# Optimization experiments

Hardware: AMD Instinct MI355X
Metric: run time of the kernel (lower is better)

## Reference

```python
import jax, jax.numpy as jnp
import numpy as np

N = 100000
E = 1600000
IN = 128
HID = 128
OUT = 40
EPS = 1e-5
NEG_SLOPE = 0.2


def _gat_layer(x, src, dst, W, a_src, a_dst, b, heads, out_dim):
    # x: [N, in]; W: [in, heads*out_dim]; a_src/a_dst: [heads, out_dim]; b: [heads*out_dim]
    n = x.shape[0]
    h = (x @ W).reshape(n, heads, out_dim)                      # [N, H, D]
    al_s = jnp.sum(h * a_src, axis=-1)                          # [N, H]
    al_d = jnp.sum(h * a_dst, axis=-1)                          # [N, H]
    e = jax.nn.leaky_relu(al_s[src] + al_d[dst], NEG_SLOPE)     # [E, H]
    m = jax.ops.segment_max(e, dst, num_segments=n)             # [N, H]
    m = jnp.where(jnp.isfinite(m), m, 0.0)
    ex = jnp.exp(e - m[dst])                                    # [E, H]
    denom = jax.ops.segment_sum(ex, dst, num_segments=n)        # [N, H]
    alpha = ex / (denom[dst] + 1e-16)                           # [E, H]
    out = jax.ops.segment_sum(alpha[:, :, None] * h[src], dst, num_segments=n)  # [N, H, D]
    return out.reshape(n, heads * out_dim) + b


def _bn(h, g, beta):
    mu = jnp.mean(h, axis=0)
    var = jnp.var(h, axis=0)
    return (h - mu) * jax.lax.rsqrt(var + EPS) * g + beta


def setup_inputs() -> dict:
    key = jax.random.key(0)
    ks = jax.random.split(key, 20)
    x = jax.random.normal(ks[0], (N, IN), dtype=jnp.float32)
    edge_index = jax.random.randint(ks[1], (2, E), 0, N, dtype=jnp.int64)
    s = 0.05
    d0 = HID // 2  # 64, heads=2
    return {
        "x": x,
        "edge_index": edge_index,
        "w0": jax.random.normal(ks[2], (IN, 2 * d0), jnp.float32) * s,
        "asrc0": jax.random.normal(ks[3], (2, d0), jnp.float32) * s,
        "adst0": jax.random.normal(ks[4], (2, d0), jnp.float32) * s,
        "b0": jnp.zeros((2 * d0,), jnp.float32),
        "g0": jnp.ones((2 * d0,), jnp.float32),
        "beta0": jnp.zeros((2 * d0,), jnp.float32),
        "w1": jax.random.normal(ks[5], (HID, 2 * d0), jnp.float32) * s,
        "asrc1": jax.random.normal(ks[6], (2, d0), jnp.float32) * s,
        "adst1": jax.random.normal(ks[7], (2, d0), jnp.float32) * s,
        "b1": jnp.zeros((2 * d0,), jnp.float32),
        "g1": jnp.ones((2 * d0,), jnp.float32),
        "beta1": jnp.zeros((2 * d0,), jnp.float32),
        "w2": jax.random.normal(ks[8], (HID, OUT), jnp.float32) * s,
        "asrc2": jax.random.normal(ks[9], (1, OUT), jnp.float32) * s,
        "adst2": jax.random.normal(ks[10], (1, OUT), jnp.float32) * s,
        "b2": jnp.zeros((OUT,), jnp.float32),
    }


def reference(x, edge_index, w0, asrc0, adst0, b0, g0, beta0,
              w1, asrc1, adst1, b1, g1, beta1,
              w2, asrc2, adst2, b2):
    src, dst = edge_index[0], edge_index[1]
    d0 = HID // 2
    # layer 0: GATConv(IN, 64, heads=2) -> BN -> ReLU (dropout off in eval)
    h = _gat_layer(x, src, dst, w0, asrc0, adst0, b0, 2, d0)
    h = jax.nn.relu(_bn(h, g0, beta0))
    # layer 1
    h = _gat_layer(h, src, dst, w1, asrc1, adst1, b1, 2, d0)
    h = jax.nn.relu(_bn(h, g1, beta1))
    # layer 2: GATConv(HID, OUT, heads=1), no bn/relu
    h = _gat_layer(h, src, dst, w2, asrc2, adst2, b2, 1, OUT)
    return h
```

## Files before the change

### kernel.cpp

```cpp
#include <hip/hip_runtime.h>
#include <cstdint>


#define TILE_A 8192
#define BCAP 10240
#define NSLICE 32

typedef __attribute__((ext_vector_type(8))) short bf16x8v;
typedef __attribute__((ext_vector_type(4))) float f32x4v;
typedef __attribute__((ext_vector_type(2))) float f32x2;
typedef __attribute__((ext_vector_type(2))) unsigned int u32x2;

__device__ __forceinline__ uint32_t bf16x2_pack(float a, float b) {
  uint32_t ua = __float_as_uint(a);
  ua = (ua + 0x7FFF + ((ua >> 16) & 1)) >> 16;
  uint32_t ub = __float_as_uint(b);
  ub = (ub + 0x7FFF + ((ub >> 16) & 1)) >> 16;
  return ua | (ub << 16);
}
__device__ __forceinline__ uint16_t bf16_1(float a) {
  uint32_t ua = __float_as_uint(a);
  return (uint16_t)((ua + 0x7FFF + ((ua >> 16) & 1)) >> 16);
}
__device__ __forceinline__ f32x2 up2(uint32_t u) {
  u32x2 t = {u << 16, u & 0xFFFF0000u};
  return __builtin_bit_cast(f32x2, t);
}


__global__ __launch_bounds__(256) void bucket_hist_k(const int* __restrict__ dst,
                                                     int* __restrict__ counts,
                                                     int E, int nbA, int nbuck) {
  __shared__ int hist[256];
  int t = threadIdx.x;
  hist[t] = 0;
  __syncthreads();
  int lo = blockIdx.x * TILE_A;
  int hi = min(lo + TILE_A, E);
  for (int i = lo + t; i < hi; i += 256) atomicAdd(&hist[dst[i] >> 9], 1);
  __syncthreads();
  if (t < nbuck) counts[t * nbA + blockIdx.x] = hist[t];
}

__global__ __launch_bounds__(1024) void scan_counts_k(int* __restrict__ counts, int M,
                                                      int* __restrict__ rowptr, int N, int E) {
  __shared__ int part[1024];
  int t = threadIdx.x;
  int chunk = (M + 1023) >> 10;
  int lo = t * chunk, hi = min(lo + chunk, M);
  int s = 0;
  for (int i = lo; i < hi; ++i) s += counts[i];
  part[t] = s;
  __syncthreads();
  for (int off = 1; off < 1024; off <<= 1) {
    int u = (t >= off) ? part[t - off] : 0;
    __syncthreads();
    part[t] += u;
    __syncthreads();
  }
  int run = (t == 0) ? 0 : part[t - 1];
  for (int i = lo; i < hi; ++i) {
    int v = counts[i];
    counts[i] = run;
    run += v;
  }
  if (t == 0) rowptr[N] = E;
}

__global__ __launch_bounds__(256) void bucket_scatter_k(const int* __restrict__ src,
                                                        const int* __restrict__ dst,
                                                        const int* __restrict__ counts,
                                                        uint32_t* __restrict__ barr,
                                                        int E, int nbA, int nbuck) {
  __shared__ int cur[256];
  int t = threadIdx.x;
  if (t < nbuck) cur[t] = counts[t * nbA + blockIdx.x];
  __syncthreads();
  int lo = blockIdx.x * TILE_A;
  int hi = min(lo + TILE_A, E);
  for (int i = lo + t; i < hi; i += 256) {
    int d = dst[i];
    int b = d >> 9;
    int pos = atomicAdd(&cur[b], 1);
    barr[pos] = ((uint32_t)(d & 511) << 17) | (uint32_t)src[i];
  }
}

__global__ __launch_bounds__(256) void bucket_sort_k(const uint32_t* __restrict__ barr,
                                                     const int* __restrict__ counts,
                                                     int* __restrict__ rowptr,
                                                     int* __restrict__ csr_src,
                                                     int nbA, int nbuck, int N, int E) {
  __shared__ uint32_t ebuf[BCAP];
  __shared__ int hist[512];
  __shared__ int cur[512];
  int b = blockIdx.x;
  int t = threadIdx.x;
  int start = counts[b * nbA];
  int end = (b == nbuck - 1) ? E : counts[(b + 1) * nbA];
  int cnt = end - start;
  if (cnt > BCAP) cnt = BCAP;
  for (int i = t; i < cnt; i += 256) ebuf[i] = barr[start + i];
  for (int i = t; i < 512; i += 256) hist[i] = 0;
  __syncthreads();
  for (int i = t; i < cnt; i += 256) atomicAdd(&hist[ebuf[i] >> 17], 1);
  __syncthreads();
  if (t < 64) {
    int v[8];
    int s = 0;
#pragma unroll
    for (int k = 0; k < 8; ++k) { v[k] = hist[t * 8 + k]; s += v[k]; }
    int inc = s;
#pragma unroll
    for (int off = 1; off < 64; off <<= 1) {
      int u = __shfl_up(inc, off, 64);
      if (t >= off) inc += u;
    }
    int run = inc - s;
#pragma unroll
    for (int k = 0; k < 8; ++k) { hist[t * 8 + k] = run; run += v[k]; }
  }
  __syncthreads();
  int node0 = b << 9;
  int lim = N - node0;
  if (lim > 512) lim = 512;
  for (int i = t; i < 512; i += 256) {
    cur[i] = hist[i];
    if (i < lim) rowptr[node0 + i] = start + hist[i];
  }
  __syncthreads();
  for (int i = t; i < cnt; i += 256) {
    uint32_t e = ebuf[i];
    int ld = e >> 17;
    int pos = atomicAdd(&cur[ld], 1);
    csr_src[start + pos] = (int)(e & 0x1FFFFu);
  }
}


__global__ void w_prep_all_k(const float* __restrict__ w0, const float* __restrict__ w1,
                             const float* __restrict__ w2, uint16_t* __restrict__ wt0,
                             uint16_t* __restrict__ wt1, uint16_t* __restrict__ wt2) {
  int idx = blockIdx.x * blockDim.x + threadIdx.x;
  if (idx < 16384) {
    int n = idx >> 7, k = idx & 127;
    wt0[idx] = bf16_1(w0[k * 128 + n]);
  } else if (idx < 32768) {
    int i = idx - 16384;
    int n = i >> 7, k = i & 127;
    wt1[i] = bf16_1(w1[k * 128 + n]);
  } else if (idx < 32768 + 48 * 128) {
    int i = idx - 32768;
    int n = i >> 7, k = i & 127;
    float v = (n < 40) ? w2[k * 40 + n] : 0.f;
    wt2[i] = bf16_1(v);
  }
}

template <bool NORM, int NT, int HEADS>
__global__ __launch_bounds__(256) void gemm_mfma_k(const float* __restrict__ X,
                                                   const uint16_t* __restrict__ WT,
                                                   uint16_t* __restrict__ Hout,
                                                   const float* __restrict__ stats,
                                                   const float* __restrict__ g,
                                                   const float* __restrict__ beta,
                                                   const float* __restrict__ asrc,
                                                   const float* __restrict__ adst,
                                                   float* __restrict__ als,
                                                   float* __restrict__ ald,
                                                   int nrows, int cols) {
  __shared__ short A_lds[64 * 136];
  __shared__ float sscale[128];
  __shared__ float sbias[128];
  int tid = threadIdx.x;
  if (NORM && tid < 128) {
    float s = 0.f, s2 = 0.f;
#pragma unroll 4
    for (int sl = 0; sl < NSLICE; ++sl) {
      s += stats[sl * 256 + tid];
      s2 += stats[sl * 256 + 128 + tid];
    }
    float invn = 1.0f / (float)nrows;
    float mean = s * invn;
    float var = s2 * invn - mean * mean;
    float sc = g[tid] * rsqrtf(var + 1e-5f);
    sscale[tid] = sc;
    sbias[tid] = beta[tid] - mean * sc;
  }
  if (NORM) __syncthreads();
  int row0 = blockIdx.x * 64;
#pragma unroll
  for (int it = 0; it < 8; ++it) {
    int e = (tid + it * 256) * 4;
    int row = e >> 7;
    int kh = e & 127;
    int gr = row0 + row;
    float4 xv = make_float4(0.f, 0.f, 0.f, 0.f);
    if (gr < nrows) xv = *(const float4*)(X + (size_t)gr * 128 + kh);
    if (NORM) {
      xv.x = fmaxf(fmaf(xv.x, sscale[kh + 0], sbias[kh + 0]), 0.f);
      xv.y = fmaxf(fmaf(xv.y, sscale[kh + 1], sbias[kh + 1]), 0.f);
      xv.z = fmaxf(fmaf(xv.z, sscale[kh + 2], sbias[kh + 2]), 0.f);
      xv.w = fmaxf(fmaf(xv.w, sscale[kh + 3], sbias[kh + 3]), 0.f);
    }
    uint2 pk;
    pk.x = bf16x2_pack(xv.x, xv.y);
    pk.y = bf16x2_pack(xv.z, xv.w);
    *(uint2*)(&A_lds[row * 136 + kh]) = pk;
  }
  __syncthreads();

  int wave = tid >> 6;
  int lane = tid & 63;
  int m = lane & 15;
  int quad = lane >> 4;

  bf16x8v afrag[4];
#pragma unroll
  for (int kc = 0; kc < 4; ++kc)
    afrag[kc] = *(const bf16x8v*)(&A_lds[(wave * 16 + m) * 136 + kc * 32 + quad * 8]);

  f32x4v acc[NT];
#pragma unroll
  for (int t = 0; t < NT; ++t) acc[t] = (f32x4v){0.f, 0.f, 0.f, 0.f};

#pragma unroll
  for (int t = 0; t < NT; ++t) {
#pragma unroll
    for (int kc = 0; kc < 4; ++kc) {
      bf16x8v bfrag = *(const bf16x8v*)(WT + ((t * 16 + m) * 128 + kc * 32 + quad * 8));
      acc[t] = __builtin_amdgcn_mfma_f32_16x16x32_bf16(afrag[kc], bfrag, acc[t], 0, 0, 0);
    }
  }

#pragma unroll
  for (int t = 0; t < NT; ++t) {
    int col = t * 16 + m;
    if (col >= cols) break;
#pragma unroll
    for (int r = 0; r < 4; ++r) {
      int row = row0 + wave * 16 + quad * 4 + r;
      if (row < nrows) Hout[(size_t)row * cols + col] = bf16_1(acc[t][r]);
    }
  }

  float as_v[NT], ad_v[NT];
#pragma unroll
  for (int t = 0; t < NT; ++t) {
    int col = t * 16 + m;
    as_v[t] = (col < cols) ? asrc[col] : 0.f;
    ad_v[t] = (col < cols) ? adst[col] : 0.f;
  }
#pragma unroll
  for (int r = 0; r < 4; ++r) {
    int row = row0 + wave * 16 + quad * 4 + r;
    if (HEADS == 2) {
      float s1h0 = 0.f, s2h0 = 0.f, s1h1 = 0.f, s2h1 = 0.f;
#pragma unroll
      for (int t = 0; t < NT / 2; ++t) {
        s1h0 += acc[t][r] * as_v[t];
        s2h0 += acc[t][r] * ad_v[t];
      }
#pragma unroll
      for (int t = NT / 2; t < NT; ++t) {
        s1h1 += acc[t][r] * as_v[t];
        s2h1 += acc[t][r] * ad_v[t];
      }
#pragma unroll
      for (int off = 1; off < 16; off <<= 1) {
        s1h0 += __shfl_xor(s1h0, off, 64);
        s2h0 += __shfl_xor(s2h0, off, 64);
        s1h1 += __shfl_xor(s1h1, off, 64);
        s2h1 += __shfl_xor(s2h1, off, 64);
      }
      if (m == 0 && row < nrows) {
        ((float2*)als)[row] = make_float2(s1h0, s1h1);
        ((float2*)ald)[row] = make_float2(s2h0, s2h1);
      }
    } else {
      float s1 = 0.f, s2 = 0.f;
#pragma unroll
      for (int t = 0; t < NT; ++t) {
        s1 += acc[t][r] * as_v[t];
        s2 += acc[t][r] * ad_v[t];
      }
#pragma unroll
      for (int off = 1; off < 16; off <<= 1) {
        s1 += __shfl_xor(s1, off, 64);
        s2 += __shfl_xor(s2, off, 64);
      }
      if (m == 0 && row < nrows) {
        als[row] = s1;
        ald[row] = s2;
      }
    }
  }
}

__global__ __launch_bounds__(256) void gat_gather2_k(const int* __restrict__ rowptr,
                                                     const int* __restrict__ csr_src,
                                                     const float* __restrict__ als,
                                                     const float* __restrict__ ald,
                                                     const uint16_t* __restrict__ H,
                                                     const float* __restrict__ bias,
                                                     float* __restrict__ out,
                                                     float* __restrict__ stats, int N) {
  __shared__ float red[4][256];
  int tid = threadIdx.x;
  int wv = tid >> 6;
  int n = blockIdx.x * 4 + wv;
  int lane = tid & 63;
  int slot = lane >> 4;
  int sub = lane & 15;
  int head = sub >> 3;
  bool alive = n < N;
  int start = 0, end = 0;
  float aldn = 0.f;
  if (alive) {
    start = rowptr[n];
    end = rowptr[n + 1];
    aldn = ald[2 * n + head];
  }
  const char* hbase = (const char*)H;
  uint32_t suboff = (uint32_t)sub << 4;
  bool dlane = (sub & 7) == 0;
  f32x2 acc0 = {0.f, 0.f}, acc1 = {0.f, 0.f}, acc2 = {0.f, 0.f}, acc3 = {0.f, 0.f};
  float dsum = 0.f;
  int j = start;
  for (; j + 16 <= end; j += 16) {
    int e0 = j + slot;
    int s0 = csr_src[e0];
    int s1 = csr_src[e0 + 4];
    int s2 = csr_src[e0 + 8];
    int s3 = csr_src[e0 + 12];
    uint4 u0 = *(const uint4*)(hbase + (((uint32_t)s0 << 8) + suboff));
    uint4 u1 = *(const uint4*)(hbase + (((uint32_t)s1 << 8) + suboff));
    uint4 u2 = *(const uint4*)(hbase + (((uint32_t)s2 << 8) + suboff));
    uint4 u3 = *(const uint4*)(hbase + (((uint32_t)s3 << 8) + suboff));
    float l0 = als[2 * s0 + head] + aldn;
    float l1 = als[2 * s1 + head] + aldn;
    float l2 = als[2 * s2 + head] + aldn;
    float l3 = als[2 * s3 + head] + aldn;
    l0 = fmaxf(l0, 0.2f * l0);
    l1 = fmaxf(l1, 0.2f * l1);
    l2 = fmaxf(l2, 0.2f * l2);
    l3 = fmaxf(l3, 0.2f * l3);
    float w0 = __expf(l0), w1 = __expf(l1), w2 = __expf(l2), w3 = __expf(l3);
    if (dlane) dsum += (w0 + w1) + (w2 + w3);
    acc0 += up2(u0.x) * w0;
    acc1 += up2(u0.y) * w0;
    acc2 += up2(u0.z) * w0;
    acc3 += up2(u0.w) * w0;
    acc0 += up2(u1.x) * w1;
    acc1 += up2(u1.y) * w1;
    acc2 += up2(u1.z) * w1;
    acc3 += up2(u1.w) * w1;
    acc0 += up2(u2.x) * w2;
    acc1 += up2(u2.y) * w2;
    acc2 += up2(u2.z) * w2;
    acc3 += up2(u2.w) * w2;
    acc0 += up2(u3.x) * w3;
    acc1 += up2(u3.y) * w3;
    acc2 += up2(u3.z) * w3;
    acc3 += up2(u3.w) * w3;
  }
  for (; j < end; j += 8) {
    int last = end - 1;
    int ea = j + slot;
    int eb = ea + 4;
    int sa = csr_src[min(ea, last)];
    int sb = csr_src[min(eb, last)];
    uint4 ua = *(const uint4*)(hbase + (((uint32_t)sa << 8) + suboff));
    uint4 ub = *(const uint4*)(hbase + (((uint32_t)sb << 8) + suboff));
    float la = als[2 * sa + head] + aldn;
    float lb = als[2 * sb + head] + aldn;
    la = fmaxf(la, 0.2f * la);
    lb = fmaxf(lb, 0.2f * lb);
    float wa = (ea < end) ? __expf(la) : 0.f;
    float wb = (eb < end) ? __expf(lb) : 0.f;
    if (dlane) dsum += wa + wb;
    acc0 += up2(ua.x) * wa;
    acc1 += up2(ua.y) * wa;
    acc2 += up2(ua.z) * wa;
    acc3 += up2(ua.w) * wa;
    acc0 += up2(ub.x) * wb;
    acc1 += up2(ub.y) * wb;
    acc2 += up2(ub.z) * wb;
    acc3 += up2(ub.w) * wb;
  }
  acc0.x += __shfl_xor(acc0.x, 16, 64); acc0.x += __shfl_xor(acc0.x, 32, 64);
  acc0.y += __shfl_xor(acc0.y, 16, 64); acc0.y += __shfl_xor(acc0.y, 32, 64);
  acc1.x += __shfl_xor(acc1.x, 16, 64); acc1.x += __shfl_xor(acc1.x, 32, 64);
  acc1.y += __shfl_xor(acc1.y, 16, 64); acc1.y += __shfl_xor(acc1.y, 32, 64);
  acc2.x += __shfl_xor(acc2.x, 16, 64); acc2.x += __shfl_xor(acc2.x, 32, 64);
  acc2.y += __shfl_xor(acc2.y, 16, 64); acc2.y += __shfl_xor(acc2.y, 32, 64);
  acc3.x += __shfl_xor(acc3.x, 16, 64); acc3.x += __shfl_xor(acc3.x, 32, 64);
  acc3.y += __shfl_xor(acc3.y, 16, 64); acc3.y += __shfl_xor(acc3.y, 32, 64);
  dsum += __shfl_xor(dsum, 16, 64);
  dsum += __shfl_xor(dsum, 32, 64);
  float denom = __shfl(dsum, head << 3, 64);
  if (slot == 0) {
    float inv = 1.0f / (denom + 1e-16f);
    float4 b0 = ((const float4*)bias)[2 * sub];
    float4 b1 = ((const float4*)bias)[2 * sub + 1];
    float4 o0, o1;
    o0.x = acc0.x * inv + b0.x;
    o0.y = acc0.y * inv + b0.y;
    o0.z = acc1.x * inv + b0.z;
    o0.w = acc1.y * inv + b0.w;
    o1.x = acc2.x * inv + b1.x;
    o1.y = acc2.y * inv + b1.y;
    o1.z = acc3.x * inv + b1.z;
    o1.w = acc3.y * inv + b1.w;
    if (alive) {
      ((float4*)out)[(size_t)n * 32 + 2 * sub] = o0;
      ((float4*)out)[(size_t)n * 32 + 2 * sub + 1] = o1;
    }
    float z = alive ? 1.f : 0.f;
    int c = sub << 3;
    red[wv][c + 0] = o0.x * z;  red[wv][128 + c + 0] = o0.x * o0.x * z;
    red[wv][c + 1] = o0.y * z;  red[wv][128 + c + 1] = o0.y * o0.y * z;
    red[wv][c + 2] = o0.z * z;  red[wv][128 + c + 2] = o0.z * o0.z * z;
    red[wv][c + 3] = o0.w * z;  red[wv][128 + c + 3] = o0.w * o0.w * z;
    red[wv][c + 4] = o1.x * z;  red[wv][128 + c + 4] = o1.x * o1.x * z;
    red[wv][c + 5] = o1.y * z;  red[wv][128 + c + 5] = o1.y * o1.y * z;
    red[wv][c + 6] = o1.z * z;  red[wv][128 + c + 6] = o1.z * o1.z * z;
    red[wv][c + 7] = o1.w * z;  red[wv][128 + c + 7] = o1.w * o1.w * z;
  }
  __syncthreads();
  float v = red[0][tid] + red[1][tid] + red[2][tid] + red[3][tid];
  atomicAdd(&stats[((blockIdx.x & (NSLICE - 1)) << 8) + tid], v);
}

__global__ __launch_bounds__(256) void gat_gather1_k(const int* __restrict__ rowptr,
                                                     const int* __restrict__ csr_src,
                                                     const float* __restrict__ als,
                                                     const float* __restrict__ ald,
                                                     const uint16_t* __restrict__ H,
                                                     const float* __restrict__ bias,
                                                     float* __restrict__ out, int N) {
  int n = blockIdx.x * 4 + (threadIdx.x >> 6);
  if (n >= N) return;
  int lane = threadIdx.x & 63;
  int slot = lane / 5;
  int d = lane - slot * 5;
  bool act = slot < 12;
  int start = rowptr[n], end = rowptr[n + 1];
  float aldn = ald[n];
  const char* hbase = (const char*)H;
  uint32_t doff = (uint32_t)d << 4;
  f32x2 a0 = {0.f, 0.f}, a1 = {0.f, 0.f}, a2 = {0.f, 0.f}, a3 = {0.f, 0.f};
  float dsum = 0.f;
  for (int j = start; j < end; j += 24) {
    int last = end - 1;
    int e0 = j + slot;
    int e1 = e0 + 12;
    int s0 = act ? csr_src[min(e0, last)] : 0;
    int s1 = act ? csr_src[min(e1, last)] : 0;
    uint4 u0 = *(const uint4*)(hbase + ((uint32_t)s0 * 80u + doff));
    uint4 u1 = *(const uint4*)(hbase + ((uint32_t)s1 * 80u + doff));
    float l0 = als[s0] + aldn;
    float l1 = als[s1] + aldn;
    l0 = fmaxf(l0, 0.2f * l0);
    l1 = fmaxf(l1, 0.2f * l1);
    float w0 = (act && e0 < end) ? __expf(l0) : 0.f;
    float w1 = (act && e1 < end) ? __expf(l1) : 0.f;
    if (d == 0) dsum += w0 + w1;
    a0 += up2(u0.x) * w0;
    a1 += up2(u0.y) * w0;
    a2 += up2(u0.z) * w0;
    a3 += up2(u0.w) * w0;
    a0 += up2(u1.x) * w1;
    a1 += up2(u1.y) * w1;
    a2 += up2(u1.z) * w1;
    a3 += up2(u1.w) * w1;
  }
#define FOLD2(off)                                        \
  a0.x += __shfl(a0.x, (lane + off) & 63, 64);            \
  a0.y += __shfl(a0.y, (lane + off) & 63, 64);            \
  a1.x += __shfl(a1.x, (lane + off) & 63, 64);            \
  a1.y += __shfl(a1.y, (lane + off) & 63, 64);            \
  a2.x += __shfl(a2.x, (lane + off) & 63, 64);            \
  a2.y += __shfl(a2.y, (lane + off) & 63, 64);            \
  a3.x += __shfl(a3.x, (lane + off) & 63, 64);            \
  a3.y += __shfl(a3.y, (lane + off) & 63, 64);
  FOLD2(30)
  FOLD2(15)
  {
    float t;
    t = __shfl(a0.x, (lane + 5) & 63, 64) + __shfl(a0.x, (lane + 10) & 63, 64); a0.x += t;
    t = __shfl(a0.y, (lane + 5) & 63, 64) + __shfl(a0.y, (lane + 10) & 63, 64); a0.y += t;
    t = __shfl(a1.x, (lane + 5) & 63, 64) + __shfl(a1.x, (lane + 10) & 63, 64); a1.x += t;
    t = __shfl(a1.y, (lane + 5) & 63, 64) + __shfl(a1.y, (lane + 10) & 63, 64); a1.y += t;
    t = __shfl(a2.x, (lane + 5) & 63, 64) + __shfl(a2.x, (lane + 10) & 63, 64); a2.x += t;
    t = __shfl(a2.y, (lane + 5) & 63, 64) + __shfl(a2.y, (lane + 10) & 63, 64); a2.y += t;
    t = __shfl(a3.x, (lane + 5) & 63, 64) + __shfl(a3.x, (lane + 10) & 63, 64); a3.x += t;
    t = __shfl(a3.y, (lane + 5) & 63, 64) + __shfl(a3.y, (lane + 10) & 63, 64); a3.y += t;
  }
#undef FOLD2
#pragma unroll
  for (int off = 1; off < 64; off <<= 1) dsum += __shfl_xor(dsum, off, 64);
  if (lane < 5) {
    float inv = 1.0f / (dsum + 1e-16f);
    float4 b4a = ((const float4*)bias)[2 * d];
    float4 b4b = ((const float4*)bias)[2 * d + 1];
    float4 o0, o1;
    o0.x = a0.x * inv + b4a.x;
    o0.y = a0.y * inv + b4a.y;
    o0.z = a1.x * inv + b4a.z;
    o0.w = a1.y * inv + b4a.w;
    o1.x = a2.x * inv + b4b.x;
    o1.y = a2.y * inv + b4b.y;
    o1.z = a3.x * inv + b4b.z;
    o1.w = a3.y * inv + b4b.w;
    float* orow = out + (size_t)n * 40 + 8 * d;
    *(float4*)orow = o0;
    *(float4*)(orow + 4) = o1;
  }
}

extern "C" void kernel_launch(void* const* d_in, const int* in_sizes, int n_in,
                              void* d_out, int out_size, void* d_ws, size_t ws_size,
                              hipStream_t stream) {
  const float* x     = (const float*)d_in[0];
  const int*   ei    = (const int*)d_in[1];
  const float* w0    = (const float*)d_in[2];
  const float* asrc0 = (const float*)d_in[3];
  const float* adst0 = (const float*)d_in[4];
  const float* b0    = (const float*)d_in[5];
  const float* g0    = (const float*)d_in[6];
  const float* beta0 = (const float*)d_in[7];
  const float* w1    = (const float*)d_in[8];
  const float* asrc1 = (const float*)d_in[9];
  const float* adst1 = (const float*)d_in[10];
  const float* b1    = (const float*)d_in[11];
  const float* g1    = (const float*)d_in[12];
  const float* beta1 = (const float*)d_in[13];
  const float* w2    = (const float*)d_in[14];
  const float* asrc2 = (const float*)d_in[15];
  const float* adst2 = (const float*)d_in[16];
  const float* b2    = (const float*)d_in[17];

  const int N = in_sizes[0] / 128;
  const int E = in_sizes[1] / 2;

  const int nbuck = (N + 511) >> 9;
  const int nbA = (E + TILE_A - 1) / TILE_A;

  char* p = (char*)d_ws;
  auto carve = [&](size_t bytes) {
    char* q = p;
    p += (bytes + 255) & ~(size_t)255;
    return q;
  };
  int*      counts  = (int*)carve((size_t)nbuck * nbA * 4);
  int*      rowptr  = (int*)carve((size_t)(N + 1) * 4);
  uint32_t* barr    = (uint32_t*)carve((size_t)E * 4);
  int*      csr_src = (int*)carve((size_t)E * 4);
  float*    als     = (float*)carve((size_t)N * 2 * 4);
  float*    ald     = (float*)carve((size_t)N * 2 * 4);
  float*    stats   = (float*)carve((size_t)NSLICE * 256 * 4);
  uint16_t* wt0     = (uint16_t*)carve(128 * 128 * 2);
  uint16_t* wt1     = (uint16_t*)carve(128 * 128 * 2);
  uint16_t* wt2     = (uint16_t*)carve(48 * 128 * 2);
  uint16_t* hbuf    = (uint16_t*)carve((size_t)N * 128 * 2);
  float*    agg     = (float*)carve((size_t)N * 128 * 4);

  const int* esrc = ei;
  const int* edst = ei + E;

  bucket_hist_k<<<nbA, 256, 0, stream>>>(edst, counts, E, nbA, nbuck);
  scan_counts_k<<<1, 1024, 0, stream>>>(counts, nbuck * nbA, rowptr, N, E);
  bucket_scatter_k<<<nbA, 256, 0, stream>>>(esrc, edst, counts, barr, E, nbA, nbuck);
  bucket_sort_k<<<nbuck, 256, 0, stream>>>(barr, counts, rowptr, csr_src, nbA, nbuck, N, E);

  w_prep_all_k<<<(32768 + 48 * 128 + 255) / 256, 256, 0, stream>>>(w0, w1, w2, wt0, wt1, wt2);

  const int gemm_grid = (N + 63) / 64;
  const int node_grid = (N + 3) / 4;

  gemm_mfma_k<false, 8, 2><<<gemm_grid, 256, 0, stream>>>(x, wt0, hbuf, nullptr, nullptr,
                                                          nullptr, asrc0, adst0, als, ald,
                                                          N, 128);
  hipMemsetAsync(stats, 0, NSLICE * 256 * 4, stream);
  gat_gather2_k<<<node_grid, 256, 0, stream>>>(rowptr, csr_src, als, ald, hbuf,
                                               b0, agg, stats, N);

  gemm_mfma_k<true, 8, 2><<<gemm_grid, 256, 0, stream>>>(agg, wt1, hbuf, stats, g0, beta0,
                                                         asrc1, adst1, als, ald, N, 128);
  hipMemsetAsync(stats, 0, NSLICE * 256 * 4, stream);
  gat_gather2_k<<<node_grid, 256, 0, stream>>>(rowptr, csr_src, als, ald, hbuf,
                                               b1, agg, stats, N);

  gemm_mfma_k<true, 3, 1><<<gemm_grid, 256, 0, stream>>>(agg, wt2, hbuf, stats, g1, beta1,
                                                         asrc2, adst2, als, ald, N, 40);
  gat_gather1_k<<<node_grid, 256, 0, stream>>>(rowptr, csr_src, als, ald, hbuf,
                                               b2, (float*)d_out, N);
}
```

Measured before the change: 532.6 us.

## Process eight nodes per wave in gather and use nontemporal loads/stores

The two-head gather kernel now gives each wave 8 consecutive destination nodes instead of one. It keeps BatchNorm partial sums in registers across those nodes, so there is one LDS reduction and one stats atomic pass per block instead of per node, and the grid shrinks 8x. Streaming accesses (csr_src reads, GEMM input reads, output writes) switch to nontemporal builtins to reduce cache pollution for the gathered H rows. The cost is fewer waves in flight for hiding latency on the irregular gathers, and more serial work per wave.

```diff
diff --git a/kernel.cpp b/kernel.cpp
--- a/kernel.cpp
+++ b/kernel.cpp
@@ -195,17 +195,17 @@
     int row = e >> 7;
     int kh = e & 127;
     int gr = row0 + row;
-    float4 xv = make_float4(0.f, 0.f, 0.f, 0.f);
-    if (gr < nrows) xv = *(const float4*)(X + (size_t)gr * 128 + kh);
+    f32x4v xv = {0.f, 0.f, 0.f, 0.f};
+    if (gr < nrows) xv = __builtin_nontemporal_load((const f32x4v*)(X + (size_t)gr * 128 + kh));
     if (NORM) {
-      xv.x = fmaxf(fmaf(xv.x, sscale[kh + 0], sbias[kh + 0]), 0.f);
-      xv.y = fmaxf(fmaf(xv.y, sscale[kh + 1], sbias[kh + 1]), 0.f);
-      xv.z = fmaxf(fmaf(xv.z, sscale[kh + 2], sbias[kh + 2]), 0.f);
-      xv.w = fmaxf(fmaf(xv.w, sscale[kh + 3], sbias[kh + 3]), 0.f);
+      xv[0] = fmaxf(fmaf(xv[0], sscale[kh + 0], sbias[kh + 0]), 0.f);
+      xv[1] = fmaxf(fmaf(xv[1], sscale[kh + 1], sbias[kh + 1]), 0.f);
+      xv[2] = fmaxf(fmaf(xv[2], sscale[kh + 2], sbias[kh + 2]), 0.f);
+      xv[3] = fmaxf(fmaf(xv[3], sscale[kh + 3], sbias[kh + 3]), 0.f);
     }
     uint2 pk;
-    pk.x = bf16x2_pack(xv.x, xv.y);
-    pk.y = bf16x2_pack(xv.z, xv.w);
+    pk.x = bf16x2_pack(xv[0], xv[1]);
+    pk.y = bf16x2_pack(xv[2], xv[3]);
     *(uint2*)(&A_lds[row * 136 + kh]) = pk;
   }
   __syncthreads();
@@ -308,124 +308,137 @@
   __shared__ float red[4][256];
   int tid = threadIdx.x;
   int wv = tid >> 6;
-  int n = blockIdx.x * 4 + wv;
   int lane = tid & 63;
   int slot = lane >> 4;
   int sub = lane & 15;
   int head = sub >> 3;
-  bool alive = n < N;
-  int start = 0, end = 0;
-  float aldn = 0.f;
-  if (alive) {
-    start = rowptr[n];
-    end = rowptr[n + 1];
-    aldn = ald[2 * n + head];
-  }
   const char* hbase = (const char*)H;
   uint32_t suboff = (uint32_t)sub << 4;
   bool dlane = (sub & 7) == 0;
-  f32x2 acc0 = {0.f, 0.f}, acc1 = {0.f, 0.f}, acc2 = {0.f, 0.f}, acc3 = {0.f, 0.f};
-  float dsum = 0.f;
-  int j = start;
-  for (; j + 16 <= end; j += 16) {
-    int e0 = j + slot;
-    int s0 = csr_src[e0];
-    int s1 = csr_src[e0 + 4];
-    int s2 = csr_src[e0 + 8];
-    int s3 = csr_src[e0 + 12];
-    uint4 u0 = *(const uint4*)(hbase + (((uint32_t)s0 << 8) + suboff));
-    uint4 u1 = *(const uint4*)(hbase + (((uint32_t)s1 << 8) + suboff));
-    uint4 u2 = *(const uint4*)(hbase + (((uint32_t)s2 << 8) + suboff));
-    uint4 u3 = *(const uint4*)(hbase + (((uint32_t)s3 << 8) + suboff));
-    float l0 = als[2 * s0 + head] + aldn;
-    float l1 = als[2 * s1 + head] + aldn;
-    float l2 = als[2 * s2 + head] + aldn;
-    float l3 = als[2 * s3 + head] + aldn;
-    l0 = fmaxf(l0, 0.2f * l0);
-    l1 = fmaxf(l1, 0.2f * l1);
-    l2 = fmaxf(l2, 0.2f * l2);
-    l3 = fmaxf(l3, 0.2f * l3);
-    float w0 = __expf(l0), w1 = __expf(l1), w2 = __expf(l2), w3 = __expf(l3);
-    if (dlane) dsum += (w0 + w1) + (w2 + w3);
-    acc0 += up2(u0.x) * w0;
-    acc1 += up2(u0.y) * w0;
-    acc2 += up2(u0.z) * w0;
-    acc3 += up2(u0.w) * w0;
-    acc0 += up2(u1.x) * w1;
-    acc1 += up2(u1.y) * w1;
-    acc2 += up2(u1.z) * w1;
-    acc3 += up2(u1.w) * w1;
-    acc0 += up2(u2.x) * w2;
-    acc1 += up2(u2.y) * w2;
-    acc2 += up2(u2.z) * w2;
-    acc3 += up2(u2.w) * w2;
-    acc0 += up2(u3.x) * w3;
-    acc1 += up2(u3.y) * w3;
-    acc2 += up2(u3.z) * w3;
-    acc3 += up2(u3.w) * w3;
-  }
-  for (; j < end; j += 8) {
-    int last = end - 1;
-    int ea = j + slot;
-    int eb = ea + 4;
-    int sa = csr_src[min(ea, last)];
-    int sb = csr_src[min(eb, last)];
-    uint4 ua = *(const uint4*)(hbase + (((uint32_t)sa << 8) + suboff));
-    uint4 ub = *(const uint4*)(hbase + (((uint32_t)sb << 8) + suboff));
-    float la = als[2 * sa + head] + aldn;
-    float lb = als[2 * sb + head] + aldn;
-    la = fmaxf(la, 0.2f * la);
-    lb = fmaxf(lb, 0.2f * lb);
-    float wa = (ea < end) ? __expf(la) : 0.f;
-    float wb = (eb < end) ? __expf(lb) : 0.f;
-    if (dlane) dsum += wa + wb;
-    acc0 += up2(ua.x) * wa;
-    acc1 += up2(ua.y) * wa;
-    acc2 += up2(ua.z) * wa;
-    acc3 += up2(ua.w) * wa;
-    acc0 += up2(ub.x) * wb;
-    acc1 += up2(ub.y) * wb;
-    acc2 += up2(ub.z) * wb;
-    acc3 += up2(ub.w) * wb;
-  }
-  acc0.x += __shfl_xor(acc0.x, 16, 64); acc0.x += __shfl_xor(acc0.x, 32, 64);
-  acc0.y += __shfl_xor(acc0.y, 16, 64); acc0.y += __shfl_xor(acc0.y, 32, 64);
-  acc1.x += __shfl_xor(acc1.x, 16, 64); acc1.x += __shfl_xor(acc1.x, 32, 64);
-  acc1.y += __shfl_xor(acc1.y, 16, 64); acc1.y += __shfl_xor(acc1.y, 32, 64);
-  acc2.x += __shfl_xor(acc2.x, 16, 64); acc2.x += __shfl_xor(acc2.x, 32, 64);
-  acc2.y += __shfl_xor(acc2.y, 16, 64); acc2.y += __shfl_xor(acc2.y, 32, 64);
-  acc3.x += __shfl_xor(acc3.x, 16, 64); acc3.x += __shfl_xor(acc3.x, 32, 64);
-  acc3.y += __shfl_xor(acc3.y, 16, 64); acc3.y += __shfl_xor(acc3.y, 32, 64);
-  dsum += __shfl_xor(dsum, 16, 64);
-  dsum += __shfl_xor(dsum, 32, 64);
-  float denom = __shfl(dsum, head << 3, 64);
+  int n0 = (blockIdx.x * 4 + wv) * 8;
+  float4 b0 = ((const float4*)bias)[2 * sub];
+  float4 b1 = ((const float4*)bias)[2 * sub + 1];
+  float ss[8], sq[8];
+#pragma unroll
+  for (int k = 0; k < 8; ++k) { ss[k] = 0.f; sq[k] = 0.f; }
+
+  for (int ni = 0; ni < 8; ++ni) {
+    int n = n0 + ni;
+    bool alive = n < N;
+    int start = 0, end = 0;
+    float aldn = 0.f;
+    if (alive) {
+      start = rowptr[n];
+      end = rowptr[n + 1];
+      aldn = ald[2 * n + head];
+    }
+    f32x2 acc0 = {0.f, 0.f}, acc1 = {0.f, 0.f}, acc2 = {0.f, 0.f}, acc3 = {0.f, 0.f};
+    float dsum = 0.f;
+    int j = start;
+    for (; j + 16 <= end; j += 16) {
+      int e0 = j + slot;
+      int s0 = __builtin_nontemporal_load(csr_src + e0);
+      int s1 = __builtin_nontemporal_load(csr_src + e0 + 4);
+      int s2 = __builtin_nontemporal_load(csr_src + e0 + 8);
+      int s3 = __builtin_nontemporal_load(csr_src + e0 + 12);
+      uint4 u0 = *(const uint4*)(hbase + (((uint32_t)s0 << 8) + suboff));
+      uint4 u1 = *(const uint4*)(hbase + (((uint32_t)s1 << 8) + suboff));
+      uint4 u2 = *(const uint4*)(hbase + (((uint32_t)s2 << 8) + suboff));
+      uint4 u3 = *(const uint4*)(hbase + (((uint32_t)s3 << 8) + suboff));
+      float l0 = als[2 * s0 + head] + aldn;
+      float l1 = als[2 * s1 + head] + aldn;
+      float l2 = als[2 * s2 + head] + aldn;
+      float l3 = als[2 * s3 + head] + aldn;
+      l0 = fmaxf(l0, 0.2f * l0);
+      l1 = fmaxf(l1, 0.2f * l1);
+      l2 = fmaxf(l2, 0.2f * l2);
+      l3 = fmaxf(l3, 0.2f * l3);
+      float w0 = __expf(l0), w1 = __expf(l1), w2 = __expf(l2), w3 = __expf(l3);
+      if (dlane) dsum += (w0 + w1) + (w2 + w3);
+      acc0 += up2(u0.x) * w0;
+      acc1 += up2(u0.y) * w0;
+      acc2 += up2(u0.z) * w0;
+      acc3 += up2(u0.w) * w0;
+      acc0 += up2(u1.x) * w1;
+      acc1 += up2(u1.y) * w1;
+      acc2 += up2(u1.z) * w1;
+      acc3 += up2(u1.w) * w1;
+      acc0 += up2(u2.x) * w2;
+      acc1 += up2(u2.y) * w2;
+      acc2 += up2(u2.z) * w2;
+      acc3 += up2(u2.w) * w2;
+      acc0 += up2(u3.x) * w3;
+      acc1 += up2(u3.y) * w3;
+      acc2 += up2(u3.z) * w3;
+      acc3 += up2(u3.w) * w3;
+    }
+    for (; j < end; j += 8) {
+      int last = end - 1;
+      int ea = j + slot;
+      int eb = ea + 4;
+      int sa = csr_src[min(ea, last)];
+      int sb = csr_src[min(eb, last)];
+      uint4 ua = *(const uint4*)(hbase + (((uint32_t)sa << 8) + suboff));
+      uint4 ub = *(const uint4*)(hbase + (((uint32_t)sb << 8) + suboff));
+      float la = als[2 * sa + head] + aldn;
+      float lb = als[2 * sb + head] + aldn;
+      la = fmaxf(la, 0.2f * la);
+      lb = fmaxf(lb, 0.2f * lb);
+      float wa = (ea < end) ? __expf(la) : 0.f;
+      float wb = (eb < end) ? __expf(lb) : 0.f;
+      if (dlane) dsum += wa + wb;
+      acc0 += up2(ua.x) * wa;
+      acc1 += up2(ua.y) * wa;
+      acc2 += up2(ua.z) * wa;
+      acc3 += up2(ua.w) * wa;
+      acc0 += up2(ub.x) * wb;
+      acc1 += up2(ub.y) * wb;
+      acc2 += up2(ub.z) * wb;
+      acc3 += up2(ub.w) * wb;
+    }
+    acc0.x += __shfl_xor(acc0.x, 16, 64); acc0.x += __shfl_xor(acc0.x, 32, 64);
+    acc0.y += __shfl_xor(acc0.y, 16, 64); acc0.y += __shfl_xor(acc0.y, 32, 64);
+    acc1.x += __shfl_xor(acc1.x, 16, 64); acc1.x += __shfl_xor(acc1.x, 32, 64);
+    acc1.y += __shfl_xor(acc1.y, 16, 64); acc1.y += __shfl_xor(acc1.y, 32, 64);
+    acc2.x += __shfl_xor(acc2.x, 16, 64); acc2.x += __shfl_xor(acc2.x, 32, 64);
+    acc2.y += __shfl_xor(acc2.y, 16, 64); acc2.y += __shfl_xor(acc2.y, 32, 64);
+    acc3.x += __shfl_xor(acc3.x, 16, 64); acc3.x += __shfl_xor(acc3.x, 32, 64);
+    acc3.y += __shfl_xor(acc3.y, 16, 64); acc3.y += __shfl_xor(acc3.y, 32, 64);
+    dsum += __shfl_xor(dsum, 16, 64);
+    dsum += __shfl_xor(dsum, 32, 64);
+    float denom = __shfl(dsum, head << 3, 64);
+    if (slot == 0 && alive) {
+      float inv = 1.0f / (denom + 1e-16f);
+      f32x4v o0, o1;
+      o0[0] = acc0.x * inv + b0.x;
+      o0[1] = acc0.y * inv + b0.y;
+      o0[2] = acc1.x * inv + b0.z;
+      o0[3] = acc1.y * inv + b0.w;
+      o1[0] = acc2.x * inv + b1.x;
+      o1[1] = acc2.y * inv + b1.y;
+      o1[2] = acc3.x * inv + b1.z;
+      o1[3] = acc3.y * inv + b1.w;
+      float* orow = out + (size_t)n * 128 + 8 * sub;
+      __builtin_nontemporal_store(o0, (f32x4v*)orow);
+      __builtin_nontemporal_store(o1, (f32x4v*)(orow + 4));
+      ss[0] += o0[0]; sq[0] += o0[0] * o0[0];
+      ss[1] += o0[1]; sq[1] += o0[1] * o0[1];
+      ss[2] += o0[2]; sq[2] += o0[2] * o0[2];
+      ss[3] += o0[3]; sq[3] += o0[3] * o0[3];
+      ss[4] += o1[0]; sq[4] += o1[0] * o1[0];
+      ss[5] += o1[1]; sq[5] += o1[1] * o1[1];
+      ss[6] += o1[2]; sq[6] += o1[2] * o1[2];
+      ss[7] += o1[3]; sq[7] += o1[3] * o1[3];
+    }
+  }
+
   if (slot == 0) {
-    float inv = 1.0f / (denom + 1e-16f);
-    float4 b0 = ((const float4*)bias)[2 * sub];
-    float4 b1 = ((const float4*)bias)[2 * sub + 1];
-    float4 o0, o1;
-    o0.x = acc0.x * inv + b0.x;
-    o0.y = acc0.y * inv + b0.y;
-    o0.z = acc1.x * inv + b0.z;
-    o0.w = acc1.y * inv + b0.w;
-    o1.x = acc2.x * inv + b1.x;
-    o1.y = acc2.y * inv + b1.y;
-    o1.z = acc3.x * inv + b1.z;
-    o1.w = acc3.y * inv + b1.w;
-    if (alive) {
-      ((float4*)out)[(size_t)n * 32 + 2 * sub] = o0;
-      ((float4*)out)[(size_t)n * 32 + 2 * sub + 1] = o1;
-    }
-    float z = alive ? 1.f : 0.f;
     int c = sub << 3;
-    red[wv][c + 0] = o0.x * z;  red[wv][128 + c + 0] = o0.x * o0.x * z;
-    red[wv][c + 1] = o0.y * z;  red[wv][128 + c + 1] = o0.y * o0.y * z;
-    red[wv][c + 2] = o0.z * z;  red[wv][128 + c + 2] = o0.z * o0.z * z;
-    red[wv][c + 3] = o0.w * z;  red[wv][128 + c + 3] = o0.w * o0.w * z;
-    red[wv][c + 4] = o1.x * z;  red[wv][128 + c + 4] = o1.x * o1.x * z;
-    red[wv][c + 5] = o1.y * z;  red[wv][128 + c + 5] = o1.y * o1.y * z;
-    red[wv][c + 6] = o1.z * z;  red[wv][128 + c + 6] = o1.z * o1.z * z;
-    red[wv][c + 7] = o1.w * z;  red[wv][128 + c + 7] = o1.w * o1.w * z;
+#pragma unroll
+    for (int k = 0; k < 8; ++k) {
+      red[wv][c + k] = ss[k];
+      red[wv][128 + c + k] = sq[k];
+    }
   }
   __syncthreads();
   float v = red[0][tid] + red[1][tid] + red[2][tid] + red[3][tid];
@@ -455,8 +468,8 @@
     int last = end - 1;
     int e0 = j + slot;
     int e1 = e0 + 12;
-    int s0 = act ? csr_src[min(e0, last)] : 0;
-    int s1 = act ? csr_src[min(e1, last)] : 0;
+    int s0 = act ? __builtin_nontemporal_load(csr_src + min(e0, last)) : 0;
+    int s1 = act ? __builtin_nontemporal_load(csr_src + min(e1, last)) : 0;
     uint4 u0 = *(const uint4*)(hbase + ((uint32_t)s0 * 80u + doff));
     uint4 u1 = *(const uint4*)(hbase + ((uint32_t)s1 * 80u + doff));
     float l0 = als[s0] + aldn;
@@ -504,18 +517,18 @@
     float inv = 1.0f / (dsum + 1e-16f);
     float4 b4a = ((const float4*)bias)[2 * d];
     float4 b4b = ((const float4*)bias)[2 * d + 1];
-    float4 o0, o1;
-    o0.x = a0.x * inv + b4a.x;
-    o0.y = a0.y * inv + b4a.y;
-    o0.z = a1.x * inv + b4a.z;
-    o0.w = a1.y * inv + b4a.w;
-    o1.x = a2.x * inv + b4b.x;
-    o1.y = a2.y * inv + b4b.y;
-    o1.z = a3.x * inv + b4b.z;
-    o1.w = a3.y * inv + b4b.w;
+    f32x4v o0, o1;
+    o0[0] = a0.x * inv + b4a.x;
+    o0[1] = a0.y * inv + b4a.y;
+    o0[2] = a1.x * inv + b4a.z;
+    o0[3] = a1.y * inv + b4a.w;
+    o1[0] = a2.x * inv + b4b.x;
+    o1[1] = a2.y * inv + b4b.y;
+    o1[2] = a3.x * inv + b4b.z;
+    o1[3] = a3.y * inv + b4b.w;
     float* orow = out + (size_t)n * 40 + 8 * d;
-    *(float4*)orow = o0;
-    *(float4*)(orow + 4) = o1;
+    __builtin_nontemporal_store(o0, (f32x4v*)orow);
+    __builtin_nontemporal_store(o1, (f32x4v*)(orow + 4));
   }
 }
 
@@ -577,20 +590,21 @@
   w_prep_all_k<<<(32768 + 48 * 128 + 255) / 256, 256, 0, stream>>>(w0, w1, w2, wt0, wt1, wt2);
 
   const int gemm_grid = (N + 63) / 64;
+  const int g2_grid = (N + 31) / 32;
   const int node_grid = (N + 3) / 4;
 
   gemm_mfma_k<false, 8, 2><<<gemm_grid, 256, 0, stream>>>(x, wt0, hbuf, nullptr, nullptr,
                                                           nullptr, asrc0, adst0, als, ald,
                                                           N, 128);
   hipMemsetAsync(stats, 0, NSLICE * 256 * 4, stream);
-  gat_gather2_k<<<node_grid, 256, 0, stream>>>(rowptr, csr_src, als, ald, hbuf,
-                                               b0, agg, stats, N);
+  gat_gather2_k<<<g2_grid, 256, 0, stream>>>(rowptr, csr_src, als, ald, hbuf,
+                                             b0, agg, stats, N);
 
   gemm_mfma_k<true, 8, 2><<<gemm_grid, 256, 0, stream>>>(agg, wt1, hbuf, stats, g0, beta0,
                                                          asrc1, adst1, als, ald, N, 128);
   hipMemsetAsync(stats, 0, NSLICE * 256 * 4, stream);
-  gat_gather2_k<<<node_grid, 256, 0, stream>>>(rowptr, csr_src, als, ald, hbuf,
-                                               b1, agg, stats, N);
+  gat_gather2_k<<<g2_grid, 256, 0, stream>>>(rowptr, csr_src, als, ald, hbuf,
+                                             b1, agg, stats, N);
 
   gemm_mfma_k<true, 3, 1><<<gemm_grid, 256, 0, stream>>>(agg, wt2, hbuf, stats, g1, beta1,
                                                          asrc2, adst2, als, ald, N, 40);
```

Result: no change. 540.3 us (+1.4%).
